# Optimization experiments

Measured on AMD Instinct MI355X. Metric: run time of the kernel, lower is better.

The kernel has to match this reference:

```python
import jax, jax.numpy as jnp
import numpy as np

B, NQ, NKV, D, H = 8, 1024, 2048, 1024, 16
HD = D // H
EPS = 1e-5  # torch F.layer_norm default


def make_rope(n, hd):
    # standard RoPE tables: theta=10000, freqs repeated to head_dim via half/half layout
    inv = 1.0 / (10000.0 ** (np.arange(0, hd, 2, dtype=np.float64) / hd))
    ang = np.arange(n, dtype=np.float64)[:, None] * inv[None, :]  # [n, hd/2]
    ang = np.concatenate([ang, ang], axis=-1)  # [n, hd]
    return jnp.asarray(np.cos(ang), jnp.float32), jnp.asarray(np.sin(ang), jnp.float32)


def setup_inputs() -> dict:
    key = jax.random.key(0)
    ks = jax.random.split(key, 8)
    s = 1.0 / np.sqrt(D)
    q_cos, q_sin = make_rope(NQ, HD)
    kv_cos, kv_sin = make_rope(NKV, HD)
    return {
        "q_in": jax.random.normal(ks[0], (B, NQ, D), jnp.float32),
        "kv_in": jax.random.normal(ks[1], (B, NKV, D), jnp.float32),
        "q_cos": q_cos, "q_sin": q_sin,
        "kv_cos": kv_cos, "kv_sin": kv_sin,
        "Wq": jax.random.normal(ks[2], (D, D), jnp.float32) * s,
        "bq": jnp.zeros((D,), jnp.float32),
        "Wk": jax.random.normal(ks[3], (D, D), jnp.float32) * s,
        "bk": jnp.zeros((D,), jnp.float32),
        "Wv": jax.random.normal(ks[4], (D, D), jnp.float32) * s,
        "bv": jnp.zeros((D,), jnp.float32),
        "Wo": jax.random.normal(ks[5], (D, D), jnp.float32) * s,
        "bo": jnp.zeros((D,), jnp.float32),
    }


def _layer_norm(x):
    mu = jnp.mean(x, axis=-1, keepdims=True)
    var = jnp.mean(jnp.square(x - mu), axis=-1, keepdims=True)
    return (x - mu) * jax.lax.rsqrt(var + EPS)


def _to_multihead(x):
    # [B, N, D] -> [B, H, N, hd]
    b, n, _ = x.shape
    return x.reshape(b, n, H, HD).transpose(0, 2, 1, 3)


def _rotate_half(x):
    x1, x2 = jnp.split(x, 2, axis=-1)
    return jnp.concatenate([-x2, x1], axis=-1)


def _rope(x, cos, sin):
    # x: [B, H, N, hd]; cos/sin: [N, hd]
    return x * cos[None, None] + _rotate_half(x) * sin[None, None]


def reference(q_in, kv_in, q_cos, q_sin, kv_cos, kv_sin,
              Wq, bq, Wk, bk, Wv, bv, Wo, bo):
    qn = _layer_norm(q_in)
    kvn = _layer_norm(kv_in)
    q = _to_multihead(qn @ Wq.T + bq)
    k = _to_multihead(kvn @ Wk.T + bk)
    v = _to_multihead(kvn @ Wv.T + bv)
    q = _rope(q, q_cos, q_sin)
    k = _rope(k, kv_cos, kv_sin)
    # SDPA
    scores = jnp.einsum('bhqd,bhkd->bhqk', q, k) / np.sqrt(HD).astype(np.float32)
    attn = jax.nn.softmax(scores, axis=-1)
    out = jnp.einsum('bhqk,bhkd->bhqd', attn, v)  # [B, H, NQ, hd]
    out = out.transpose(0, 2, 1, 3).reshape(q_in.shape[0], q_in.shape[1], D)
    return out @ Wo.T + bo
```

## Files before the change

kernel.cpp:

```cpp
#include <hip/hip_runtime.h>
#include <stdint.h>
#include <stddef.h>

#define B_   8
#define NQ_  1024
#define NKV_ 2048
#define D_   1024
#define H_   16
#define HD_  64

typedef __bf16 bf16;
typedef __bf16 bf16x4 __attribute__((ext_vector_type(4)));
typedef __bf16 bf16x8 __attribute__((ext_vector_type(8)));
typedef float  f32x4  __attribute__((ext_vector_type(4)));

__device__ __forceinline__ void gload_lds16(const void* g, void* l) {
  __builtin_amdgcn_global_load_lds((const __attribute__((address_space(1))) void*)g,
                                   (__attribute__((address_space(3))) void*)l, 16, 0, 0);
}

__global__ void cvt_w_kernel(const float* __restrict__ w0, const float* __restrict__ w1,
                             const float* __restrict__ w2, const float* __restrict__ w3,
                             bf16* __restrict__ o0, bf16* __restrict__ o1,
                             bf16* __restrict__ o2, bf16* __restrict__ o3) {
  const float* s; bf16* d;
  switch (blockIdx.y) {
    case 0: s = w0; d = o0; break;
    case 1: s = w1; d = o1; break;
    case 2: s = w2; d = o2; break;
    default: s = w3; d = o3; break;
  }
  int i = (blockIdx.x * 256 + threadIdx.x) * 4;
  float4 v = *(const float4*)(s + i);
  bf16x4 t = { (bf16)v.x, (bf16)v.y, (bf16)v.z, (bf16)v.w };
  *(bf16x4*)(d + i) = t;
}

__global__ void ln_bf16_kernel(const float* __restrict__ x, bf16* __restrict__ y) {
  int w = threadIdx.x >> 6, l = threadIdx.x & 63;
  int row = blockIdx.x * 4 + w;
  const float* xr = x + (size_t)row * D_;
  float4 v[4];
#pragma unroll
  for (int k = 0; k < 4; ++k) v[k] = *(const float4*)(xr + k * 256 + l * 4);
  float s = 0.f, ss = 0.f;
#pragma unroll
  for (int k = 0; k < 4; ++k) {
    s  += v[k].x + v[k].y + v[k].z + v[k].w;
    ss += v[k].x * v[k].x + v[k].y * v[k].y + v[k].z * v[k].z + v[k].w * v[k].w;
  }
#pragma unroll
  for (int m = 1; m < 64; m <<= 1) { s += __shfl_xor(s, m); ss += __shfl_xor(ss, m); }
  float mu = s * (1.f / D_);
  float var = ss * (1.f / D_) - mu * mu;
  float rs = rsqrtf(var + 1e-5f);
  bf16* yr = y + (size_t)row * D_;
#pragma unroll
  for (int k = 0; k < 4; ++k) {
    bf16x4 t = { (bf16)((v[k].x - mu) * rs), (bf16)((v[k].y - mu) * rs),
                 (bf16)((v[k].z - mu) * rs), (bf16)((v[k].w - mu) * rs) };
    *(bf16x4*)(yr + k * 256 + l * 4) = t;
  }
}

__device__ __forceinline__ int swz64(int row, int slot) {
  return row * 64 + ((slot ^ ((row >> 1) & 3)) << 4);
}

template<int EPI>
__global__ __launch_bounds__(256)
void gemm_bt(const bf16* __restrict__ A, const bf16* __restrict__ Bw,
             const float* __restrict__ bias,
             const float* __restrict__ cosT, const float* __restrict__ sinT,
             void* __restrict__ outp, int seq_shift) {
  __shared__ bf16 As[2][128 * 32];
  __shared__ bf16 Bs[2][128 * 32];
  const int tid = threadIdx.x;
  const int w = tid >> 6, l = tid & 63;
  const int wr = w >> 1, wc = w & 1;
  const int lg = l >> 4, lr = l & 15;
  const int mbase = blockIdx.y * 128, nbase = blockIdx.x * 128;

  f32x4 acc[4][4] = {};

  auto stage = [&](int k0, int buf) {
#pragma unroll
    for (int i = 0; i < 2; ++i) {
      int S = i * 256 + tid;
      int row = S >> 2, st = S & 3;
      int gs = st ^ ((row >> 1) & 3);
      gload_lds16((const char*)(A + ((size_t)(mbase + row) * 1024 + k0)) + gs * 16,
                  (char*)&As[buf][0] + (i * 256 + w * 64) * 16);
    }
#pragma unroll
    for (int i = 0; i < 2; ++i) {
      int S = i * 256 + tid;
      int row = S >> 2, st = S & 3;
      int gs = st ^ ((row >> 1) & 3);
      gload_lds16((const char*)(Bw + ((size_t)(nbase + row) * 1024 + k0)) + gs * 16,
                  (char*)&Bs[buf][0] + (i * 256 + w * 64) * 16);
    }
  };

  stage(0, 0);
  __syncthreads();
  for (int it = 0; it < 32; ++it) {
    int buf = it & 1;
    if (it + 1 < 32) stage((it + 1) * 32, buf ^ 1);
    bf16x8 af[4], bfr[4];
#pragma unroll
    for (int fr = 0; fr < 4; ++fr)
      af[fr] = *(const bf16x8*)((const char*)&As[buf][0] + swz64(wr * 64 + fr * 16 + lr, lg));
#pragma unroll
    for (int fc = 0; fc < 4; ++fc)
      bfr[fc] = *(const bf16x8*)((const char*)&Bs[buf][0] + swz64(wc * 64 + fc * 16 + lr, lg));
#pragma unroll
    for (int fr = 0; fr < 4; ++fr)
#pragma unroll
      for (int fc = 0; fc < 4; ++fc)
        acc[fr][fc] = __builtin_amdgcn_mfma_f32_16x16x32_bf16(af[fr], bfr[fc], acc[fr][fc], 0, 0, 0);
    __syncthreads();
  }

#pragma unroll
  for (int fr = 0; fr < 4; ++fr)
#pragma unroll
    for (int r = 0; r < 4; ++r) {
      int mrow = mbase + wr * 64 + fr * 16 + lg * 4 + r;
#pragma unroll
      for (int fc = 0; fc < 4; ++fc) {
        int n = nbase + wc * 64 + fc * 16 + lr;
        float x = acc[fr][fc][r];
        if (EPI == 0) {
          float xb  = x + bias[n];
          float xpb = acc[fr][fc ^ 2][r] + bias[n ^ 32];
          int d = n & 63, h = n >> 6;
          int seqN = 1 << seq_shift;
          int pos = mrow & (seqN - 1), bi = mrow >> seq_shift;
          float c = cosT[pos * 64 + d], s2 = sinT[pos * 64 + d];
          float yv = xb * c + ((d < 32) ? -xpb : xpb) * s2;
          ((bf16*)outp)[((size_t)(bi * H_ + h) * seqN + pos) * 64 + d] = (bf16)yv;
        } else if (EPI == 2) {
          int bi = n >> 11, kp = n & (NKV_ - 1);
          ((bf16*)outp)[(size_t)bi * (1024 * NKV_) + (size_t)mrow * NKV_ + kp] =
              (bf16)(x + bias[mrow]);
        } else {
          ((float*)outp)[(size_t)mrow * 1024 + n] = x + bias[n];
        }
      }
    }
}

__device__ __forceinline__ int swz128(int row, int slot) {
  return row * 128 + ((slot ^ (row & 7)) << 4);
}

__global__ __launch_bounds__(256)
void attn_kernel(const bf16* __restrict__ Qh, const bf16* __restrict__ Kh,
                 const bf16* __restrict__ Vt, bf16* __restrict__ Ao) {
  __shared__ bf16 Ks[2][64 * 64];
  __shared__ bf16 Vs[2][64 * 64];
  __shared__ bf16 Ps[4][16 * 64];
  const int tid = threadIdx.x, w = tid >> 6, l = tid & 63;
  const int lg = l >> 4, lr = l & 15;
  const int bh = blockIdx.y;
  const int q0 = blockIdx.x * 64;

  bf16x8 aq[2];
  {
    const bf16* qrow = Qh + ((size_t)bh * NQ_ + q0 + w * 16 + lr) * 64;
#pragma unroll
    for (int ks = 0; ks < 2; ++ks) aq[ks] = *(const bf16x8*)(qrow + ks * 32 + lg * 8);
  }

  const char* Kbase = (const char*)(Kh + (size_t)bh * NKV_ * 64);
  const char* Vbase = (const char*)(Vt + (size_t)bh * 64 * NKV_);

  auto stageKV = [&](int t, int buf) {
#pragma unroll
    for (int i = 0; i < 2; ++i) {
      int S = i * 256 + tid;
      int row = S >> 3, st = S & 7;
      int gs = st ^ (row & 7);
      gload_lds16(Kbase + (size_t)(t * 64 + row) * 128 + gs * 16,
                  (char*)&Ks[buf][0] + (i * 256 + w * 64) * 16);
    }
#pragma unroll
    for (int i = 0; i < 2; ++i) {
      int S = i * 256 + tid;
      int row = S >> 3, st = S & 7;
      int gs = st ^ (row & 7);
      gload_lds16(Vbase + (size_t)row * (NKV_ * 2) + (size_t)t * 128 + gs * 16,
                  (char*)&Vs[buf][0] + (i * 256 + w * 64) * 16);
    }
  };

  float mrun[4], lrun[4];
  f32x4 oacc[4] = {};
#pragma unroll
  for (int r = 0; r < 4; ++r) { mrun[r] = -1e30f; lrun[r] = 0.f; }

  stageKV(0, 0);
  __syncthreads();

  const float LOG2E = 1.44269504f;
  for (int t = 0; t < NKV_ / 64; ++t) {
    int buf = t & 1;
    if (t + 1 < NKV_ / 64) stageKV(t + 1, buf ^ 1);

    f32x4 sacc[4] = {};
    __builtin_amdgcn_s_setprio(1);
#pragma unroll
    for (int nt = 0; nt < 4; ++nt)
#pragma unroll
      for (int ks = 0; ks < 2; ++ks) {
        bf16x8 kf = *(const bf16x8*)((const char*)&Ks[buf][0] + swz128(nt * 16 + lr, ks * 4 + lg));
        sacc[nt] = __builtin_amdgcn_mfma_f32_16x16x32_bf16(aq[ks], kf, sacc[nt], 0, 0, 0);
      }
    __builtin_amdgcn_s_setprio(0);

    float p[4][4];
#pragma unroll
    for (int nt = 0; nt < 4; ++nt)
#pragma unroll
      for (int r = 0; r < 4; ++r) p[nt][r] = sacc[nt][r] * 0.125f;

    float alpha[4];
#pragma unroll
    for (int r = 0; r < 4; ++r) {
      float mt = fmaxf(fmaxf(p[0][r], p[1][r]), fmaxf(p[2][r], p[3][r]));
#pragma unroll
      for (int msk = 1; msk < 16; msk <<= 1) mt = fmaxf(mt, __shfl_xor(mt, msk));
      float mn = fmaxf(mrun[r], mt);
      alpha[r] = exp2f((mrun[r] - mn) * LOG2E);
      mrun[r] = mn;
      float rs = 0.f;
#pragma unroll
      for (int nt = 0; nt < 4; ++nt) { p[nt][r] = exp2f((p[nt][r] - mn) * LOG2E); rs += p[nt][r]; }
#pragma unroll
      for (int msk = 1; msk < 16; msk <<= 1) rs += __shfl_xor(rs, msk);
      lrun[r] = lrun[r] * alpha[r] + rs;
#pragma unroll
      for (int dt = 0; dt < 4; ++dt) oacc[dt][r] *= alpha[r];
    }

    {
      char* Pw = (char*)&Ps[w][0];
#pragma unroll
      for (int nt = 0; nt < 4; ++nt)
#pragma unroll
        for (int r = 0; r < 4; ++r) {
          int qr = lg * 4 + r, kc = nt * 16 + lr;
          int off = qr * 128 + ((((kc >> 3) ^ (qr & 7))) << 4) + (kc & 7) * 2;
          *(bf16*)(Pw + off) = (bf16)p[nt][r];
        }
    }

    bf16x8 pf[2];
#pragma unroll
    for (int ks = 0; ks < 2; ++ks)
      pf[ks] = *(const bf16x8*)((const char*)&Ps[w][0] + swz128(lr, ks * 4 + lg));
    __builtin_amdgcn_s_setprio(1);
#pragma unroll
    for (int dt = 0; dt < 4; ++dt)
#pragma unroll
      for (int ks = 0; ks < 2; ++ks) {
        bf16x8 vf = *(const bf16x8*)((const char*)&Vs[buf][0] + swz128(dt * 16 + lr, ks * 4 + lg));
        oacc[dt] = __builtin_amdgcn_mfma_f32_16x16x32_bf16(pf[ks], vf, oacc[dt], 0, 0, 0);
      }
    __builtin_amdgcn_s_setprio(0);
    __syncthreads();
  }

  int b = bh >> 4, h = bh & 15;
#pragma unroll
  for (int r = 0; r < 4; ++r) {
    float inv = 1.f / lrun[r];
    int qpos = q0 + w * 16 + lg * 4 + r;
#pragma unroll
    for (int dt = 0; dt < 4; ++dt) {
      int col = h * 64 + dt * 16 + lr;
      Ao[((size_t)b * NQ_ + qpos) * D_ + col] = (bf16)(oacc[dt][r] * inv);
    }
  }
}

extern "C" void kernel_launch(void* const* d_in, const int* in_sizes, int n_in,
                              void* d_out, int out_size, void* d_ws, size_t ws_size,
                              hipStream_t stream) {
  (void)in_sizes; (void)n_in; (void)out_size; (void)ws_size;
  const float* q_in   = (const float*)d_in[0];
  const float* kv_in  = (const float*)d_in[1];
  const float* q_cos  = (const float*)d_in[2];
  const float* q_sin  = (const float*)d_in[3];
  const float* kv_cos = (const float*)d_in[4];
  const float* kv_sin = (const float*)d_in[5];
  const float* Wq = (const float*)d_in[6];
  const float* bq = (const float*)d_in[7];
  const float* Wk = (const float*)d_in[8];
  const float* bk = (const float*)d_in[9];
  const float* Wv = (const float*)d_in[10];
  const float* bv = (const float*)d_in[11];
  const float* Wo = (const float*)d_in[12];
  const float* bo = (const float*)d_in[13];

  char* ws = (char*)d_ws;
  bf16* qn  = (bf16*)ws;              ws += (size_t)B_ * NQ_ * D_ * 2;
  bf16* kvn = (bf16*)ws;              ws += (size_t)B_ * NKV_ * D_ * 2;
  bf16* wqb = (bf16*)ws;              ws += (size_t)D_ * D_ * 2;
  bf16* wkb = (bf16*)ws;              ws += (size_t)D_ * D_ * 2;
  bf16* wvb = (bf16*)ws;              ws += (size_t)D_ * D_ * 2;
  bf16* wob = (bf16*)ws;              ws += (size_t)D_ * D_ * 2;
  bf16* Qh  = (bf16*)ws;              ws += (size_t)B_ * H_ * NQ_ * 64 * 2;
  bf16* Kh  = (bf16*)ws;              ws += (size_t)B_ * H_ * NKV_ * 64 * 2;
  bf16* Vt  = (bf16*)ws;              ws += (size_t)B_ * H_ * 64 * NKV_ * 2;
  bf16* Ao  = qn;

  cvt_w_kernel<<<dim3(1024, 4), 256, 0, stream>>>(Wq, Wk, Wv, Wo, wqb, wkb, wvb, wob);
  ln_bf16_kernel<<<(B_ * NQ_) / 4, 256, 0, stream>>>(q_in, qn);
  ln_bf16_kernel<<<(B_ * NKV_) / 4, 256, 0, stream>>>(kv_in, kvn);

  gemm_bt<0><<<dim3(D_ / 128, (B_ * NQ_) / 128), 256, 0, stream>>>(
      qn, wqb, bq, q_cos, q_sin, (void*)Qh, 10);
  gemm_bt<0><<<dim3(D_ / 128, (B_ * NKV_) / 128), 256, 0, stream>>>(
      kvn, wkb, bk, kv_cos, kv_sin, (void*)Kh, 11);
  gemm_bt<2><<<dim3((B_ * NKV_) / 128, D_ / 128), 256, 0, stream>>>(
      wvb, kvn, bv, nullptr, nullptr, (void*)Vt, 0);

  attn_kernel<<<dim3(NQ_ / 64, B_ * H_), 256, 0, stream>>>(Qh, Kh, Vt, Ao);

  gemm_bt<3><<<dim3(D_ / 128, (B_ * NQ_) / 128), 256, 0, stream>>>(
      Ao, wob, bo, nullptr, nullptr, d_out, 0);
}
```

Measured before the change: 648.9 us.

## Restructure attention around 32x32x16 MFMA with transposed S and 128-query blocks

Rewrites the flash-attention kernel to use 32x32x16 bf16 MFMAs computing S^T (K as A operand), so each lane owns one query row. The softmax reduction then needs only a single cross-half shuffle instead of 4-step butterflies, and the scale is folded into one exp2 argument. Each block now handles 128 queries, so every staged K/V tile is reused across twice as many queries. The 1D grid is remapped so neighbouring blocks share a head (bh) for better L2 locality. The cost is more accumulator registers (two f32x16 each for S and O) and a larger P buffer in shared memory, which may reduce occupancy.

Result: faster. 565.1 us (-12.9%).

```diff
diff --git a/kernel.cpp b/kernel.cpp
--- a/kernel.cpp
+++ b/kernel.cpp
@@ -13,10 +13,20 @@
 typedef __bf16 bf16x4 __attribute__((ext_vector_type(4)));
 typedef __bf16 bf16x8 __attribute__((ext_vector_type(8)));
 typedef float  f32x4  __attribute__((ext_vector_type(4)));
+typedef float  f32x16 __attribute__((ext_vector_type(16)));
+typedef unsigned int u32;
+typedef u32 u32x2 __attribute__((ext_vector_type(2)));
+typedef unsigned short u16;
 
 __device__ __forceinline__ void gload_lds16(const void* g, void* l) {
   __builtin_amdgcn_global_load_lds((const __attribute__((address_space(1))) void*)g,
                                    (__attribute__((address_space(3))) void*)l, 16, 0, 0);
+}
+
+__device__ __forceinline__ u32 pack2(float a, float b) {
+  u16 ua = __builtin_bit_cast(u16, (bf16)a);
+  u16 ub = __builtin_bit_cast(u16, (bf16)b);
+  return (u32)ua | ((u32)ub << 16);
 }
 
 __global__ void cvt_w_kernel(const float* __restrict__ w0, const float* __restrict__ w1,
@@ -160,17 +170,20 @@
                  const bf16* __restrict__ Vt, bf16* __restrict__ Ao) {
   __shared__ bf16 Ks[2][64 * 64];
   __shared__ bf16 Vs[2][64 * 64];
-  __shared__ bf16 Ps[4][16 * 64];
-  const int tid = threadIdx.x, w = tid >> 6, l = tid & 63;
-  const int lg = l >> 4, lr = l & 15;
-  const int bh = blockIdx.y;
-  const int q0 = blockIdx.x * 64;
-
-  bf16x8 aq[2];
+  __shared__ bf16 Ps[4][32 * 64];
+  const int tid = threadIdx.x, wq = tid >> 6, l = tid & 63;
+  const int q31 = l & 31, h = l >> 5;
+
+  int bid = blockIdx.x;
+  int vid = (bid & 7) * 128 + (bid >> 3);
+  const int bh = vid >> 3;
+  const int q0 = (vid & 7) * 128;
+
+  bf16x8 aq[4];
   {
-    const bf16* qrow = Qh + ((size_t)bh * NQ_ + q0 + w * 16 + lr) * 64;
-#pragma unroll
-    for (int ks = 0; ks < 2; ++ks) aq[ks] = *(const bf16x8*)(qrow + ks * 32 + lg * 8);
+    const bf16* qrow = Qh + ((size_t)bh * NQ_ + q0 + wq * 32 + q31) * 64;
+#pragma unroll
+    for (int kt = 0; kt < 4; ++kt) aq[kt] = *(const bf16x8*)(qrow + kt * 16 + h * 8);
   }
 
   const char* Kbase = (const char*)(Kh + (size_t)bh * NKV_ * 64);
@@ -183,7 +196,7 @@
       int row = S >> 3, st = S & 7;
       int gs = st ^ (row & 7);
       gload_lds16(Kbase + (size_t)(t * 64 + row) * 128 + gs * 16,
-                  (char*)&Ks[buf][0] + (i * 256 + w * 64) * 16);
+                  (char*)&Ks[buf][0] + (i * 256 + wq * 64) * 16);
     }
 #pragma unroll
     for (int i = 0; i < 2; ++i) {
@@ -191,98 +204,101 @@
       int row = S >> 3, st = S & 7;
       int gs = st ^ (row & 7);
       gload_lds16(Vbase + (size_t)row * (NKV_ * 2) + (size_t)t * 128 + gs * 16,
-                  (char*)&Vs[buf][0] + (i * 256 + w * 64) * 16);
+                  (char*)&Vs[buf][0] + (i * 256 + wq * 64) * 16);
     }
   };
 
-  float mrun[4], lrun[4];
-  f32x4 oacc[4] = {};
-#pragma unroll
-  for (int r = 0; r < 4; ++r) { mrun[r] = -1e30f; lrun[r] = 0.f; }
+  float mrun = -3.0e38f, lrun = 0.f;
+  f32x16 oaccT[2] = {};
 
   stageKV(0, 0);
   __syncthreads();
 
-  const float LOG2E = 1.44269504f;
+  const float SC = 0.125f * 1.44269504f;
+  char* Pw = (char*)&Ps[wq][0];
+
   for (int t = 0; t < NKV_ / 64; ++t) {
     int buf = t & 1;
     if (t + 1 < NKV_ / 64) stageKV(t + 1, buf ^ 1);
 
-    f32x4 sacc[4] = {};
+    f32x16 st[2] = {};
     __builtin_amdgcn_s_setprio(1);
 #pragma unroll
-    for (int nt = 0; nt < 4; ++nt)
-#pragma unroll
-      for (int ks = 0; ks < 2; ++ks) {
-        bf16x8 kf = *(const bf16x8*)((const char*)&Ks[buf][0] + swz128(nt * 16 + lr, ks * 4 + lg));
-        sacc[nt] = __builtin_amdgcn_mfma_f32_16x16x32_bf16(aq[ks], kf, sacc[nt], 0, 0, 0);
+    for (int kvt = 0; kvt < 2; ++kvt)
+#pragma unroll
+      for (int kt = 0; kt < 4; ++kt) {
+        bf16x8 kf = *(const bf16x8*)((const char*)&Ks[buf][0] +
+                                     swz128(kvt * 32 + q31, kt * 2 + h));
+        st[kvt] = __builtin_amdgcn_mfma_f32_32x32x16_bf16(kf, aq[kt], st[kvt], 0, 0, 0);
       }
     __builtin_amdgcn_s_setprio(0);
 
-    float p[4][4];
-#pragma unroll
-    for (int nt = 0; nt < 4; ++nt)
-#pragma unroll
-      for (int r = 0; r < 4; ++r) p[nt][r] = sacc[nt][r] * 0.125f;
-
-    float alpha[4];
-#pragma unroll
-    for (int r = 0; r < 4; ++r) {
-      float mt = fmaxf(fmaxf(p[0][r], p[1][r]), fmaxf(p[2][r], p[3][r]));
-#pragma unroll
-      for (int msk = 1; msk < 16; msk <<= 1) mt = fmaxf(mt, __shfl_xor(mt, msk));
-      float mn = fmaxf(mrun[r], mt);
-      alpha[r] = exp2f((mrun[r] - mn) * LOG2E);
-      mrun[r] = mn;
-      float rs = 0.f;
-#pragma unroll
-      for (int nt = 0; nt < 4; ++nt) { p[nt][r] = exp2f((p[nt][r] - mn) * LOG2E); rs += p[nt][r]; }
-#pragma unroll
-      for (int msk = 1; msk < 16; msk <<= 1) rs += __shfl_xor(rs, msk);
-      lrun[r] = lrun[r] * alpha[r] + rs;
-#pragma unroll
-      for (int dt = 0; dt < 4; ++dt) oacc[dt][r] *= alpha[r];
-    }
-
-    {
-      char* Pw = (char*)&Ps[w][0];
-#pragma unroll
-      for (int nt = 0; nt < 4; ++nt)
-#pragma unroll
-        for (int r = 0; r < 4; ++r) {
-          int qr = lg * 4 + r, kc = nt * 16 + lr;
-          int off = qr * 128 + ((((kc >> 3) ^ (qr & 7))) << 4) + (kc & 7) * 2;
-          *(bf16*)(Pw + off) = (bf16)p[nt][r];
-        }
-    }
-
-    bf16x8 pf[2];
-#pragma unroll
-    for (int ks = 0; ks < 2; ++ks)
-      pf[ks] = *(const bf16x8*)((const char*)&Ps[w][0] + swz128(lr, ks * 4 + lg));
+    float ms = st[0][0];
+#pragma unroll
+    for (int i = 1; i < 16; ++i) ms = fmaxf(ms, st[0][i]);
+#pragma unroll
+    for (int i = 0; i < 16; ++i) ms = fmaxf(ms, st[1][i]);
+    ms = fmaxf(ms, __shfl_xor(ms, 32));
+    float mn = fmaxf(mrun, ms);
+    float alpha = exp2f((mrun - mn) * SC);
+    mrun = mn;
+    float bterm = mn * SC;
+    float rs = 0.f;
+#pragma unroll
+    for (int kvt = 0; kvt < 2; ++kvt)
+#pragma unroll
+      for (int i = 0; i < 16; ++i) {
+        float p = exp2f(st[kvt][i] * SC - bterm);
+        st[kvt][i] = p;
+        rs += p;
+      }
+    rs += __shfl_xor(rs, 32);
+    lrun = lrun * alpha + rs;
+#pragma unroll
+    for (int dt = 0; dt < 2; ++dt)
+#pragma unroll
+      for (int i = 0; i < 16; ++i) oaccT[dt][i] *= alpha;
+
+#pragma unroll
+    for (int kvt = 0; kvt < 2; ++kvt)
+#pragma unroll
+      for (int g = 0; g < 4; ++g) {
+        u32x2 dv = { pack2(st[kvt][g * 4 + 0], st[kvt][g * 4 + 1]),
+                     pack2(st[kvt][g * 4 + 2], st[kvt][g * 4 + 3]) };
+        *(u32x2*)(Pw + swz128(q31, kvt * 4 + g) + h * 8) = dv;
+      }
+
+    bf16x8 pf[4];
+#pragma unroll
+    for (int vt = 0; vt < 4; ++vt)
+      pf[vt] = *(const bf16x8*)(Pw + swz128(q31, vt * 2 + h));
+
     __builtin_amdgcn_s_setprio(1);
 #pragma unroll
-    for (int dt = 0; dt < 4; ++dt)
-#pragma unroll
-      for (int ks = 0; ks < 2; ++ks) {
-        bf16x8 vf = *(const bf16x8*)((const char*)&Vs[buf][0] + swz128(dt * 16 + lr, ks * 4 + lg));
-        oacc[dt] = __builtin_amdgcn_mfma_f32_16x16x32_bf16(pf[ks], vf, oacc[dt], 0, 0, 0);
+    for (int dt = 0; dt < 2; ++dt)
+#pragma unroll
+      for (int vt = 0; vt < 4; ++vt) {
+        bf16x8 av = *(const bf16x8*)((const char*)&Vs[buf][0] +
+                                     swz128(dt * 32 + q31, vt * 2 + h));
+        oaccT[dt] = __builtin_amdgcn_mfma_f32_32x32x16_bf16(av, pf[vt], oaccT[dt], 0, 0, 0);
       }
     __builtin_amdgcn_s_setprio(0);
     __syncthreads();
   }
 
-  int b = bh >> 4, h = bh & 15;
-#pragma unroll
-  for (int r = 0; r < 4; ++r) {
-    float inv = 1.f / lrun[r];
-    int qpos = q0 + w * 16 + lg * 4 + r;
-#pragma unroll
-    for (int dt = 0; dt < 4; ++dt) {
-      int col = h * 64 + dt * 16 + lr;
-      Ao[((size_t)b * NQ_ + qpos) * D_ + col] = (bf16)(oacc[dt][r] * inv);
-    }
-  }
+  float inv = 1.f / lrun;
+  int b = bh >> 4, hh = bh & 15;
+  bf16* orow = Ao + ((size_t)b * NQ_ + q0 + wq * 32 + q31) * D_ + hh * 64;
+#pragma unroll
+  for (int dt = 0; dt < 2; ++dt)
+#pragma unroll
+    for (int g = 0; g < 4; ++g) {
+      int d = dt * 32 + 8 * g + 4 * h;
+      u32 p0 = pack2(oaccT[dt][g * 4 + 0] * inv, oaccT[dt][g * 4 + 1] * inv);
+      u32 p1 = pack2(oaccT[dt][g * 4 + 2] * inv, oaccT[dt][g * 4 + 3] * inv);
+      *(u32*)(orow + d) = p0;
+      *(u32*)(orow + d + 2) = p1;
+    }
 }
 
 extern "C" void kernel_launch(void* const* d_in, const int* in_sizes, int n_in,
@@ -327,7 +343,7 @@
   gemm_bt<2><<<dim3((B_ * NKV_) / 128, D_ / 128), 256, 0, stream>>>(
       wvb, kvn, bv, nullptr, nullptr, (void*)Vt, 0);
 
-  attn_kernel<<<dim3(NQ_ / 64, B_ * H_), 256, 0, stream>>>(Qh, Kh, Vt, Ao);
+  attn_kernel<<<dim3((B_ * H_ * NQ_) / 128), 256, 0, stream>>>(Qh, Kh, Vt, Ao);
 
   gemm_bt<3><<<dim3(D_ / 128, (B_ * NQ_) / 128), 256, 0, stream>>>(
       Ao, wob, bo, nullptr, nullptr, d_out, 0);
```
